# Kernel optimization log

Hardware: AMD Instinct MI355X
Metric: run time of the kernel (lower is better)

The kernel has to match this reference:

```python
import jax, jax.numpy as jnp
import numpy as np

B, D, C = 4096, 256, 64  # batch, dim_embed, n_conditions
EPS = 1e-10


def setup_inputs() -> dict:
    key = jax.random.key(0)
    k1, k2, k3, k4 = jax.random.split(key, 4)
    x = jax.random.normal(k1, (B, D), dtype=jnp.float32)          # embedded_x (embeddingnet = identity)
    W = jax.random.normal(k2, (C, D, D), dtype=jnp.float32) * 0.02  # per-condition Linear weights (out,in)
    b = jax.random.normal(k3, (C, D), dtype=jnp.float32) * 0.02     # per-condition Linear biases
    c = jax.random.randint(k4, (B,), 0, C)                         # condition index per sample
    return {"x": x, "W": W, "b": b, "c": c}


def reference(x, W, b, c):
    # per-sample expert Linear: y_i = W[c_i] @ x_i + b[c_i]
    y = jnp.einsum('bij,bj->bi', W[c], x) + b[c]          # [B, D]
    # mask_norm accumulates L1 norm of the selected weight PER SAMPLE (duplicates counted)
    per_cond_l1 = jnp.sum(jnp.abs(W), axis=(1, 2))        # [C]
    mask_norm = jnp.sum(per_cond_l1[c])
    # embed_norm = global L2 (Frobenius) norm of embedded_x
    embed_norm = jnp.sqrt(jnp.sum(x * x))
    # F.normalize(p=2, dim=1, eps=1e-10): divide by max(row_norm, eps)
    row_norm = jnp.sqrt(jnp.sum(y * y, axis=1, keepdims=True))
    masked_embedding = y / jnp.maximum(row_norm, EPS)
    return (masked_embedding, mask_norm, embed_norm, x)
```

## Files before the change

kernel.cpp:

```cpp
#include <hip/hip_runtime.h>
#include <math.h>

#define B_ 4096
#define D_ 256
#define C_ 64
#define BD (B_*D_)

typedef __attribute__((ext_vector_type(8))) short bf16x8;
typedef __attribute__((ext_vector_type(4))) float f32x4;

__device__ __forceinline__ float wave_reduce_sum(float v) {
    #pragma unroll
    for (int off = 1; off < 64; off <<= 1) v += __shfl_xor(v, off);
    return v;
}

__device__ __forceinline__ unsigned cvtpk(float lo, float hi) {
    unsigned r;
    asm volatile("v_cvt_pk_bf16_f32 %0, %1, %2" : "=v"(r) : "v"(lo), "v"(hi));
    return r;
}

__global__ __launch_bounds__(256, 4) void k_main(const float* __restrict__ W,
                                                 const float* __restrict__ b,
                                                 const float* __restrict__ x,
                                                 const int* __restrict__ c,
                                                 float* __restrict__ out,
                                                 float* __restrict__ l1p,
                                                 float* __restrict__ xsqp,
                                                 int* __restrict__ cnt4) {
    int hw = blockIdx.x;
    int bid = (hw & 7) * 128 + (hw >> 3);
    int cond = bid >> 4;
    int ct = (bid >> 2) & 3;
    int sl = bid & 3;
    int tid = threadIdx.x;
    int wv = tid >> 6, lane = tid & 63;
    int g = lane >> 4, fr = lane & 15;
    int r = tid >> 2, ch = tid & 3;

    const float4* x4 = (const float4*)x;
    int xi = bid * 256 + tid;
    float4 xv = x4[xi];
    int4 cvq[4];
    #pragma unroll
    for (int t = 0; t < 4; ++t) cvq[t] = ((const int4*)c)[t * 256 + tid];
    const float4* Wt4 = (const float4*)(W + (size_t)cond * 65536) + (size_t)(ct * 64 + r) * 64 + ch * 2;
    float4 wA[2], wB[2];
    wA[0] = Wt4[0]; wA[1] = Wt4[1];
    float bias_s = b[cond * 256 + ct * 64 + wv * 16 + fr];

    __shared__ unsigned Xl[48 * 128];
    __shared__ unsigned Wl[2][64 * 20];
    __shared__ float part_x[4];
    __shared__ float part_w[4];
    __shared__ int slist[48];
    __shared__ int nlist;
    if (tid == 0) nlist = 0;

    float2* dst = (float2*)(out + BD + 2);
    dst[2 * xi]     = make_float2(xv.x, xv.y);
    dst[2 * xi + 1] = make_float2(xv.z, xv.w);
    float s = xv.x * xv.x + xv.y * xv.y + xv.z * xv.z + xv.w * xv.w;
    s = wave_reduce_sum(s);
    if (lane == 0) part_x[wv] = s;
    __syncthreads();

    #pragma unroll
    for (int t = 0; t < 4; ++t) {
        int4 q = cvq[t];
        int cc = (sl == 0) ? q.x : (sl == 1) ? q.y : (sl == 2) ? q.z : q.w;
        if (cc == cond) {
            int p = atomicAdd(&nlist, 1);
            if (p < 48) slist[p] = 4 * (t * 256 + tid) + sl;
        }
    }
    asm volatile("" : "+v"(wA[0].x), "+v"(wA[0].y), "+v"(wA[0].z), "+v"(wA[0].w),
                      "+v"(wA[1].x), "+v"(wA[1].y), "+v"(wA[1].z), "+v"(wA[1].w));
    __syncthreads();
    int n = min(nlist, 48);
    int mts = (n + 15) >> 4;
    if (tid == 0) {
        xsqp[bid] = (part_x[0] + part_x[1]) + (part_x[2] + part_x[3]);
        if (ct == 0) cnt4[cond * 4 + sl] = n;
    }

    int sgr[12];
    #pragma unroll
    for (int k = 0; k < 12; ++k) sgr[k] = slist[wv + 4 * k];
    #pragma unroll
    for (int k = 0; k < 12; ++k) {
        int u = tid + 256 * k;
        if (u < n * 64) {
            int si = u >> 6, v = u & 63;
            float4 q = x4[(size_t)sgr[k] * 64 + v];
            int off = (v * 8) ^ ((si & 7) << 4);
            Xl[si * 128 + (off >> 2)]     = cvtpk(q.x, q.y);
            Xl[si * 128 + (off >> 2) + 1] = cvtpk(q.z, q.w);
        }
    }

    float l1acc = 0.f;
    {
        uint4 pk;
        pk.x = cvtpk(wA[0].x, wA[0].y); pk.y = cvtpk(wA[0].z, wA[0].w);
        pk.z = cvtpk(wA[1].x, wA[1].y); pk.w = cvtpk(wA[1].z, wA[1].w);
        *(uint4*)(&Wl[0][r * 20 + ch * 4]) = pk;
        if (sl == 0)
            l1acc += fabsf(wA[0].x) + fabsf(wA[0].y) + fabsf(wA[0].z) + fabsf(wA[0].w)
                   + fabsf(wA[1].x) + fabsf(wA[1].y) + fabsf(wA[1].z) + fabsf(wA[1].w);
    }
    wB[0] = Wt4[8]; wB[1] = Wt4[9];
    __syncthreads();

    f32x4 acc[3];
    #pragma unroll
    for (int mt = 0; mt < 3; ++mt) acc[mt] = (f32x4){0.f, 0.f, 0.f, 0.f};

    #pragma unroll
    for (int kk = 0; kk < 8; ++kk) {
        const unsigned* Wb = Wl[kk & 1];
        bf16x8 bfr = *(const bf16x8*)(Wb + (wv * 16 + fr) * 20 + g * 4);
        #pragma unroll
        for (int mt = 0; mt < 3; ++mt) if (mt < mts) {
            int row = mt * 16 + fr;
            bf16x8 afr = *(const bf16x8*)((const char*)Xl + row * 512 + ((kk * 64 + g * 16) ^ ((row & 7) << 4)));
            acc[mt] = __builtin_amdgcn_mfma_f32_16x16x32_bf16(afr, bfr, acc[mt], 0, 0, 0);
        }
        if (kk < 7) {
            const float4* wsrc = (kk & 1) ? wA : wB;
            uint4 pk;
            pk.x = cvtpk(wsrc[0].x, wsrc[0].y); pk.y = cvtpk(wsrc[0].z, wsrc[0].w);
            pk.z = cvtpk(wsrc[1].x, wsrc[1].y); pk.w = cvtpk(wsrc[1].z, wsrc[1].w);
            *(uint4*)(&Wl[(kk + 1) & 1][r * 20 + ch * 4]) = pk;
            if (sl == 0)
                l1acc += fabsf(wsrc[0].x) + fabsf(wsrc[0].y) + fabsf(wsrc[0].z) + fabsf(wsrc[0].w)
                       + fabsf(wsrc[1].x) + fabsf(wsrc[1].y) + fabsf(wsrc[1].z) + fabsf(wsrc[1].w);
            if (kk < 6) {
                float4* wld = (kk & 1) ? wB : wA;
                wld[0] = Wt4[(kk + 2) * 8];
                wld[1] = Wt4[(kk + 2) * 8 + 1];
            }
            __syncthreads();
        }
    }

    if (sl == 0) {
        float a = wave_reduce_sum(l1acc);
        if (lane == 0) part_w[wv] = a;
    }
    __syncthreads();
    if (sl == 0 && tid == 0)
        l1p[cond * 4 + ct] = (part_w[0] + part_w[1]) + (part_w[2] + part_w[3]);

    #pragma unroll
    for (int mt = 0; mt < 3; ++mt) if (mt < mts) {
        #pragma unroll
        for (int j = 0; j < 4; ++j) {
            int row = mt * 16 + g * 4 + j;
            if (row < n) {
                int sg = slist[row];
                out[(size_t)sg * 256 + ct * 64 + wv * 16 + fr] = acc[mt][j] + bias_s;
            }
        }
    }
}

__global__ __launch_bounds__(256) void k_fin(float* __restrict__ out,
                                             const float* __restrict__ xsqp,
                                             const float* __restrict__ l1p,
                                             const int* __restrict__ cnt4) {
    int tid = threadIdx.x;
    int wv = tid >> 6, lane = tid & 63;
    if (blockIdx.x == 1024) {
        __shared__ float part[4];
        float s = 0.f;
        #pragma unroll
        for (int j = 0; j < 4; ++j) s += xsqp[tid * 4 + j];
        s = wave_reduce_sum(s);
        if (lane == 0) part[wv] = s;
        __syncthreads();
        if (tid < 64) {
            float l1 = (l1p[tid * 4 + 0] + l1p[tid * 4 + 1]) + (l1p[tid * 4 + 2] + l1p[tid * 4 + 3]);
            float cnt = (float)((cnt4[tid * 4 + 0] + cnt4[tid * 4 + 1]) + (cnt4[tid * 4 + 2] + cnt4[tid * 4 + 3]));
            float mv = l1 * cnt;
            mv = wave_reduce_sum(mv);
            if (tid == 0) out[BD] = mv;
        }
        if (tid == 0) out[BD + 1] = sqrtf((part[0] + part[1]) + (part[2] + part[3]));
        return;
    }
    int rowv = blockIdx.x * 4 + wv;
    float4* p = (float4*)out + (size_t)rowv * 64 + lane;
    float4 v = *p;
    float s = v.x * v.x + v.y * v.y + v.z * v.z + v.w * v.w;
    s = wave_reduce_sum(s);
    float inv = 1.0f / fmaxf(sqrtf(s), 1e-10f);
    v.x *= inv; v.y *= inv; v.z *= inv; v.w *= inv;
    *p = v;
}

extern "C" void kernel_launch(void* const* d_in, const int* in_sizes, int n_in,
                              void* d_out, int out_size, void* d_ws, size_t ws_size,
                              hipStream_t stream) {
    const float* x = (const float*)d_in[0];
    const float* W = (const float*)d_in[1];
    const float* b = (const float*)d_in[2];
    const int*   c = (const int*)d_in[3];
    float* out = (float*)d_out;

    float* xsqp = (float*)d_ws;
    float* l1p  = xsqp + 1024;
    int*   cnt4 = (int*)(l1p + 256);

    k_main<<<1024, 256, 0, stream>>>(W, b, x, c, out, l1p, xsqp, cnt4);
    k_fin<<<1025, 256, 0, stream>>>(out, xsqp, l1p, cnt4);
}
```

Baseline: 18.40 us.

## Load weight B-fragments directly into registers, dropping LDS staging and barriers

Each lane now loads the exact W elements its MFMA B-fragment needs straight from global memory into registers and converts them to bf16 in place. This removes the double-buffered LDS weight tile and the per-k-step __syncthreads that staging required. Register prefetching of the next k-slice is kept, and the L1-norm accumulation moves into the main loop. Global access becomes less coalesced (each lane reads two float4 per row at 1KB row stride), which may cost memory efficiency in exchange for removing barrier and LDS traffic.

```diff
diff --git a/kernel.cpp b/kernel.cpp
--- a/kernel.cpp
+++ b/kernel.cpp
@@ -37,7 +37,6 @@
     int tid = threadIdx.x;
     int wv = tid >> 6, lane = tid & 63;
     int g = lane >> 4, fr = lane & 15;
-    int r = tid >> 2, ch = tid & 3;
 
     const float4* x4 = (const float4*)x;
     int xi = bid * 256 + tid;
@@ -45,13 +44,12 @@
     int4 cvq[4];
     #pragma unroll
     for (int t = 0; t < 4; ++t) cvq[t] = ((const int4*)c)[t * 256 + tid];
-    const float4* Wt4 = (const float4*)(W + (size_t)cond * 65536) + (size_t)(ct * 64 + r) * 64 + ch * 2;
-    float4 wA[2], wB[2];
-    wA[0] = Wt4[0]; wA[1] = Wt4[1];
+    const float4* Wp = (const float4*)(W + (size_t)cond * 65536 + (size_t)(ct * 64 + wv * 16 + fr) * 256) + g * 2;
+    float4 w0a = Wp[0], w0b = Wp[1];
+    float4 w1a = Wp[8], w1b = Wp[9];
     float bias_s = b[cond * 256 + ct * 64 + wv * 16 + fr];
 
     __shared__ unsigned Xl[48 * 128];
-    __shared__ unsigned Wl[2][64 * 20];
     __shared__ float part_x[4];
     __shared__ float part_w[4];
     __shared__ int slist[48];
@@ -75,8 +73,6 @@
             if (p < 48) slist[p] = 4 * (t * 256 + tid) + sl;
         }
     }
-    asm volatile("" : "+v"(wA[0].x), "+v"(wA[0].y), "+v"(wA[0].z), "+v"(wA[0].w),
-                      "+v"(wA[1].x), "+v"(wA[1].y), "+v"(wA[1].z), "+v"(wA[1].w));
     __syncthreads();
     int n = min(nlist, 48);
     int mts = (n + 15) >> 4;
@@ -99,50 +95,30 @@
             Xl[si * 128 + (off >> 2) + 1] = cvtpk(q.z, q.w);
         }
     }
-
-    float l1acc = 0.f;
-    {
-        uint4 pk;
-        pk.x = cvtpk(wA[0].x, wA[0].y); pk.y = cvtpk(wA[0].z, wA[0].w);
-        pk.z = cvtpk(wA[1].x, wA[1].y); pk.w = cvtpk(wA[1].z, wA[1].w);
-        *(uint4*)(&Wl[0][r * 20 + ch * 4]) = pk;
-        if (sl == 0)
-            l1acc += fabsf(wA[0].x) + fabsf(wA[0].y) + fabsf(wA[0].z) + fabsf(wA[0].w)
-                   + fabsf(wA[1].x) + fabsf(wA[1].y) + fabsf(wA[1].z) + fabsf(wA[1].w);
-    }
-    wB[0] = Wt4[8]; wB[1] = Wt4[9];
     __syncthreads();
 
     f32x4 acc[3];
     #pragma unroll
     for (int mt = 0; mt < 3; ++mt) acc[mt] = (f32x4){0.f, 0.f, 0.f, 0.f};
+    float l1acc = 0.f;
 
     #pragma unroll
     for (int kk = 0; kk < 8; ++kk) {
-        const unsigned* Wb = Wl[kk & 1];
-        bf16x8 bfr = *(const bf16x8*)(Wb + (wv * 16 + fr) * 20 + g * 4);
+        bf16x8 bfr;
+        unsigned* bp = (unsigned*)&bfr;
+        bp[0] = cvtpk(w0a.x, w0a.y); bp[1] = cvtpk(w0a.z, w0a.w);
+        bp[2] = cvtpk(w0b.x, w0b.y); bp[3] = cvtpk(w0b.z, w0b.w);
+        if (sl == 0)
+            l1acc += fabsf(w0a.x) + fabsf(w0a.y) + fabsf(w0a.z) + fabsf(w0a.w)
+                   + fabsf(w0b.x) + fabsf(w0b.y) + fabsf(w0b.z) + fabsf(w0b.w);
         #pragma unroll
         for (int mt = 0; mt < 3; ++mt) if (mt < mts) {
             int row = mt * 16 + fr;
             bf16x8 afr = *(const bf16x8*)((const char*)Xl + row * 512 + ((kk * 64 + g * 16) ^ ((row & 7) << 4)));
             acc[mt] = __builtin_amdgcn_mfma_f32_16x16x32_bf16(afr, bfr, acc[mt], 0, 0, 0);
         }
-        if (kk < 7) {
-            const float4* wsrc = (kk & 1) ? wA : wB;
-            uint4 pk;
-            pk.x = cvtpk(wsrc[0].x, wsrc[0].y); pk.y = cvtpk(wsrc[0].z, wsrc[0].w);
-            pk.z = cvtpk(wsrc[1].x, wsrc[1].y); pk.w = cvtpk(wsrc[1].z, wsrc[1].w);
-            *(uint4*)(&Wl[(kk + 1) & 1][r * 20 + ch * 4]) = pk;
-            if (sl == 0)
-                l1acc += fabsf(wsrc[0].x) + fabsf(wsrc[0].y) + fabsf(wsrc[0].z) + fabsf(wsrc[0].w)
-                       + fabsf(wsrc[1].x) + fabsf(wsrc[1].y) + fabsf(wsrc[1].z) + fabsf(wsrc[1].w);
-            if (kk < 6) {
-                float4* wld = (kk & 1) ? wB : wA;
-                wld[0] = Wt4[(kk + 2) * 8];
-                wld[1] = Wt4[(kk + 2) * 8 + 1];
-            }
-            __syncthreads();
-        }
+        w0a = w1a; w0b = w1b;
+        if (kk < 6) { w1a = Wp[(kk + 2) * 8]; w1b = Wp[(kk + 2) * 8 + 1]; }
     }
 
     if (sl == 0) {
```

Result: slower. 21.11 us (+14.7%).
